# Performance work log

Measured on AMD Instinct MI355X. Metric: run time of the kernel, lower is better.

Reference implementation:

```python
import jax, jax.numpy as jnp
import numpy as np

H = 12  # num_heads

def _alibi_bias(num_heads, n, dtype):
    # slopes: ratio**i for i in 1..H, ratio = 2**(-8/H)
    ratio = 2.0 ** (-8.0 / num_heads)
    slopes = ratio ** jnp.arange(1, num_heads + 1, dtype=jnp.float32)  # [H]
    pos = jnp.arange(n)
    rel = jnp.abs(pos[None, :] - pos[:, None]).astype(jnp.float32)  # [N,N]
    return (-slopes[:, None, None] * rel[None]).astype(dtype)  # [H,N,N]

def setup_inputs() -> dict:
    key = jax.random.key(0)
    ks = jax.random.split(key, 5)
    B, N, C = 16, 1024, 768
    s = 0.02
    return {
        "x": jax.random.normal(ks[0], (B, N, C), jnp.float32),
        "w_qkv": jax.random.normal(ks[1], (3 * C, C), jnp.float32) * s,
        "b_qkv": jax.random.normal(ks[2], (3 * C,), jnp.float32) * s,
        "w_proj": jax.random.normal(ks[3], (C, C), jnp.float32) * s,
        "b_proj": jax.random.normal(ks[4], (C,), jnp.float32) * s,
    }

def reference(x, w_qkv, b_qkv, w_proj, b_proj):
    B, N, C = x.shape
    D = C // H
    scale = D ** -0.5
    qkv = x @ w_qkv.T + b_qkv                       # [B,N,3C]
    qkv = qkv.reshape(B, N, 3, H, D)
    q = qkv[:, :, 0].transpose(0, 2, 1, 3)          # [B,H,N,D]
    k = qkv[:, :, 1].transpose(0, 2, 1, 3)
    v = qkv[:, :, 2].transpose(0, 2, 1, 3)
    bias = _alibi_bias(H, N, x.dtype)               # [H,N,N]
    scores = jnp.einsum('bhnd,bhmd->bhnm', q, k) * scale + bias[None]
    attn = jax.nn.softmax(scores, axis=-1)
    out = jnp.einsum('bhnm,bhmd->bhnd', attn, v)    # [B,H,N,D]
    out = out.transpose(0, 2, 1, 3).reshape(B, N, C)
    return out @ w_proj.T + b_proj
```

## Files before the change

### kernel.cpp

```cpp
#include <hip/hip_runtime.h>


typedef unsigned short u16;
typedef unsigned int u32;
typedef __attribute__((ext_vector_type(8))) short short8;
typedef __attribute__((ext_vector_type(4))) float f32x4;

__device__ __forceinline__ u16 f2bf(float f) {
    u32 u = __float_as_uint(f);
    u32 r = u + 0x7FFFu + ((u >> 16) & 1u);
    return (u16)(r >> 16);
}

__device__ __forceinline__ f32x4 mfma16(short8 a, short8 b, f32x4 c) {
    return __builtin_amdgcn_mfma_f32_16x16x32_bf16(a, b, c, 0, 0, 0);
}
__device__ __forceinline__ u32 cvtpk_bf16(float lo, float hi) {
    u32 r;
    asm("v_cvt_pk_bf16_f32 %0, %1, %2" : "=v"(r) : "v"(lo), "v"(hi));
    return r;
}

typedef __attribute__((address_space(1))) const unsigned int gu32_t;
typedef __attribute__((address_space(3))) unsigned int su32_t;
__device__ __forceinline__ void gl16(const u16* g, u16* s) {
    __builtin_amdgcn_global_load_lds((gu32_t*)g, (su32_t*)s, 16, 0, 0);
}

__global__ void cvt_all(const float* __restrict__ x, const float* __restrict__ wq,
                        const float* __restrict__ wp, u16* __restrict__ Xb,
                        u16* __restrict__ Wqkvb, u16* __restrict__ Wprojb) {
    int i = blockIdx.x * blockDim.x + threadIdx.x;
    int stride = gridDim.x * blockDim.x;
    for (int idx = i; idx < 3735552; idx += stride) {
        const float* src;
        u16* dst;
        int k;
        if (idx < 3145728) { src = x; dst = Xb; k = idx; }
        else if (idx < 3588096) { src = wq; dst = Wqkvb; k = idx - 3145728; }
        else { src = wp; dst = Wprojb; k = idx - 3588096; }
        float4 v = *(const float4*)(src + (size_t)k * 4);
        ushort4 o;
        o.x = f2bf(v.x); o.y = f2bf(v.y); o.z = f2bf(v.z); o.w = f2bf(v.w);
        *(ushort4*)(dst + (size_t)k * 4) = o;
    }
}

template <int EPI>
__global__ __launch_bounds__(256) void gemm_nt(
    const u16* __restrict__ A, const u16* __restrict__ Bw,
    const float* __restrict__ bias, u16* __restrict__ outb, float* __restrict__ outf,
    int nTilesN)
{
    constexpr int K = 768;
    constexpr int nkt = K / 32;
    __shared__ __align__(16) u16 lA[3][128 * 32];
    __shared__ __align__(16) u16 lB[3][128 * 32];

    int tid = threadIdx.x;
    int bid = blockIdx.x;
    int nwg = gridDim.x;
    int cpx = nwg >> 3;
    int swz = (bid & 7) * cpx + (bid >> 3);
    int bm = swz / nTilesN;
    int bn = swz - bm * nTilesN;
    int m0 = bm * 128, n0 = bn * 128;

    int sr = tid >> 2;
    int sc = (tid & 3) << 3;
    const u16* pA = A + (size_t)(m0 + sr) * K + sc;
    const u16* pB = Bw + (size_t)(n0 + sr) * K + sc;
    int lo = tid * 8;

    gl16(pA, &lA[0][lo]);
    gl16(pA + (size_t)64 * K, &lA[0][lo + 2048]);
    gl16(pB, &lB[0][lo]);
    gl16(pB + (size_t)64 * K, &lB[0][lo + 2048]);
    gl16(pA + 32, &lA[1][lo]);
    gl16(pA + (size_t)64 * K + 32, &lA[1][lo + 2048]);
    gl16(pB + 32, &lB[1][lo]);
    gl16(pB + (size_t)64 * K + 32, &lB[1][lo + 2048]);

    int w = tid >> 6, lane = tid & 63;
    int wr = (w >> 1) << 6, wc = (w & 1) << 6;
    int fq = lane >> 4, fr = lane & 15;
    f32x4 acc[4][4] = {};

    for (int kt = 0; kt < nkt; ++kt) {
        int cur = kt % 3;
        if (kt < nkt - 1) { asm volatile("s_waitcnt vmcnt(4)" ::: "memory"); }
        else              { asm volatile("s_waitcnt vmcnt(0)" ::: "memory"); }
        __builtin_amdgcn_sched_barrier(0);
        __builtin_amdgcn_s_barrier();
        __builtin_amdgcn_sched_barrier(0);
        if (kt + 2 < nkt) {
            int nx = (kt + 2) % 3;
            const u16* qA = pA + (kt + 2) * 32;
            const u16* qB = pB + (kt + 2) * 32;
            gl16(qA, &lA[nx][lo]);
            gl16(qA + (size_t)64 * K, &lA[nx][lo + 2048]);
            gl16(qB, &lB[nx][lo]);
            gl16(qB + (size_t)64 * K, &lB[nx][lo + 2048]);
        }
        short8 af[4], bfr[4];
#pragma unroll
        for (int i = 0; i < 4; ++i)
            af[i] = *(const short8*)&lA[cur][(wr + i * 16 + fr) * 32 + fq * 8];
#pragma unroll
        for (int j = 0; j < 4; ++j)
            bfr[j] = *(const short8*)&lB[cur][(wc + j * 16 + fr) * 32 + fq * 8];
        __builtin_amdgcn_s_setprio(1);
#pragma unroll
        for (int i = 0; i < 4; ++i)
#pragma unroll
            for (int j = 0; j < 4; ++j)
                acc[i][j] = mfma16(af[i], bfr[j], acc[i][j]);
        __builtin_amdgcn_s_setprio(0);
    }

    if (EPI == 0) {
        int nbase = n0 + wc;
        int s = nbase / 768;
        int hh = (nbase % 768) >> 6;
        int b = m0 >> 10;
        int i0 = (m0 & 1023) + wr;
        u16* obase = outb + (((size_t)s * 16 + b) * 12 + hh) * 1024 * 64;
#pragma unroll
        for (int j = 0; j < 4; ++j) {
            float bval = bias[nbase + j * 16 + fr];
            int d = j * 16 + fr;
#pragma unroll
            for (int i = 0; i < 4; ++i) {
                int r0 = i0 + i * 16 + fq * 4;
#pragma unroll
                for (int r = 0; r < 4; ++r)
                    obase[(size_t)(r0 + r) * 64 + d] = f2bf(acc[i][j][r] + bval);
            }
        }
    } else {
#pragma unroll
        for (int j = 0; j < 4; ++j) {
            int col = n0 + wc + j * 16 + fr;
            float bval = bias[col];
#pragma unroll
            for (int i = 0; i < 4; ++i) {
                int row0 = m0 + wr + i * 16 + fq * 4;
#pragma unroll
                for (int r = 0; r < 4; ++r)
                    outf[(size_t)(row0 + r) * 768 + col] = acc[i][j][r] + bval;
            }
        }
    }
}

__global__ __launch_bounds__(256) void attn_alibi(
    const u16* __restrict__ QKV, u16* __restrict__ att)
{
    int g = blockIdx.x;
    int xcd = g & 7;
    int idx = g >> 3;
    int qt = idx & 15;
    int bh = xcd * 24 + (idx >> 4);
    int h = bh % 12;
    int b = bh / 12;
    int q0 = qt * 64;
    const u16* Qg = QKV + (size_t)bh * 65536;
    const u16* Kg = QKV + (size_t)(192 + bh) * 65536;
    const u16* Vg = QKV + (size_t)(384 + bh) * 65536;

    __shared__ __align__(16) u16 Qs[64][72];
    __shared__ __align__(16) u16 Ks[64][72];
    __shared__ __align__(16) u16 Vt[64][72];
    __shared__ __align__(16) u16 Ps[64][72];

    int tid = threadIdx.x, w = tid >> 6, lane = tid & 63;
    int fq = lane >> 4, fr = lane & 15;

    for (int c = tid; c < 512; c += 256) {
        int r = c >> 3, d = (c & 7) * 8;
        *(uint4*)&Qs[r][d] = *(const uint4*)(Qg + (size_t)(q0 + r) * 64 + d);
    }
    __syncthreads();
    short8 aq0 = *(const short8*)&Qs[w * 16 + fr][fq * 8];
    short8 aq1 = *(const short8*)&Qs[w * 16 + fr][32 + fq * 8];

    const float C1 = 0.125f * 1.44269504f;
    float c2 = __builtin_amdgcn_exp2f(-(2.0f / 3.0f) * (float)(h + 1)) * 1.44269504f;
    int distThr = (int)(40.0f / c2);
    int lo_kv = q0 - 63 - distThr;
    int hi_kv = q0 + 63 + distThr;
    int t_lo = (lo_kv <= 0) ? 0 : (lo_kv >> 6);
    int t_hi = (hi_kv >= 1023) ? 15 : (hi_kv >> 6);

    int sr0 = tid >> 3;
    int sr1 = sr0 + 32;
    int sc = (tid & 7) * 8;
    int vswz = (tid & 7) << 3;

    uint4 kr0 = *(const uint4*)(Kg + (size_t)(t_lo * 64 + sr0) * 64 + sc);
    uint4 kr1 = *(const uint4*)(Kg + (size_t)(t_lo * 64 + sr1) * 64 + sc);
    uint4 vr0 = *(const uint4*)(Vg + (size_t)(t_lo * 64 + sr0) * 64 + sc);
    uint4 vr1 = *(const uint4*)(Vg + (size_t)(t_lo * 64 + sr1) * 64 + sc);

    float di = (float)(q0 + w * 16 + fr - fq * 4);
    float lsum = 0.f;
    f32x4 acc[4] = {};

    for (int it = t_lo; it <= t_hi; ++it) {
        __syncthreads();
        *(uint4*)&Ks[sr0][sc] = kr0;
        *(uint4*)&Ks[sr1][sc] = kr1;
        {
            const u16* v0 = (const u16*)&vr0;
            const u16* v1 = (const u16*)&vr1;
#pragma unroll
            for (int jj = 0; jj < 8; ++jj) {
                Vt[sc + jj][sr0 ^ vswz] = v0[jj];
                Vt[sc + jj][sr1 ^ vswz] = v1[jj];
            }
        }
        __syncthreads();

        if (it < t_hi) {
            int kvn = (it + 1) * 64;
            kr0 = *(const uint4*)(Kg + (size_t)(kvn + sr0) * 64 + sc);
            kr1 = *(const uint4*)(Kg + (size_t)(kvn + sr1) * 64 + sc);
            vr0 = *(const uint4*)(Vg + (size_t)(kvn + sr0) * 64 + sc);
            vr1 = *(const uint4*)(Vg + (size_t)(kvn + sr1) * 64 + sc);
        }

        f32x4 sfr[4];
        __builtin_amdgcn_s_setprio(1);
#pragma unroll
        for (int ct = 0; ct < 4; ++ct) {
            short8 bk0 = *(const short8*)&Ks[ct * 16 + fr][fq * 8];
            short8 bk1 = *(const short8*)&Ks[ct * 16 + fr][32 + fq * 8];
            f32x4 s0 = {0.f, 0.f, 0.f, 0.f};
            s0 = mfma16(bk0, aq0, s0);
            s0 = mfma16(bk1, aq1, s0);
            sfr[ct] = s0;
        }
        __builtin_amdgcn_s_setprio(0);

        float dkv = di - (float)(it * 64);
#pragma unroll
        for (int ct = 0; ct < 4; ++ct) {
#pragma unroll
            for (int rp = 0; rp < 2; ++rp) {
                float t0 = dkv - (float)(ct * 16 + rp * 2);
                float e0 = __builtin_amdgcn_exp2f(fmaf(sfr[ct][rp * 2], C1, -c2 * fabsf(t0)));
                float e1 = __builtin_amdgcn_exp2f(fmaf(sfr[ct][rp * 2 + 1], C1, -c2 * fabsf(t0 - 1.0f)));
                lsum += e0 + e1;
                *(u32*)&Ps[w * 16 + fr][ct * 16 + fq * 4 + rp * 2] = cvtpk_bf16(e0, e1);
            }
        }

        short8 pa0 = *(const short8*)&Ps[w * 16 + fr][fq * 8];
        short8 pa1 = *(const short8*)&Ps[w * 16 + fr][32 + fq * 8];
        __builtin_amdgcn_s_setprio(1);
#pragma unroll
        for (int dt = 0; dt < 4; ++dt) {
            int row = dt * 16 + fr;
            int swzr = (row >> 3) << 3;
            short8 bv0 = *(const short8*)&Vt[row][(fq * 8) ^ swzr];
            short8 bv1 = *(const short8*)&Vt[row][(32 + fq * 8) ^ swzr];
            acc[dt] = mfma16(pa0, bv0, acc[dt]);
            acc[dt] = mfma16(pa1, bv1, acc[dt]);
        }
        __builtin_amdgcn_s_setprio(0);
    }

    float l = lsum;
    l += __shfl_xor(l, 16);
    l += __shfl_xor(l, 32);
    float rlo = 1.0f / l;
    float rl[4];
#pragma unroll
    for (int r = 0; r < 4; ++r)
        rl[r] = __shfl(rlo, fq * 4 + r);

#pragma unroll
    for (int dt = 0; dt < 4; ++dt)
#pragma unroll
        for (int r = 0; r < 4; ++r) {
            int ig = q0 + w * 16 + fq * 4 + r;
            att[((size_t)(b * 1024 + ig) * 12 + h) * 64 + dt * 16 + fr] =
                (u16)cvtpk_bf16(acc[dt][r] * rl[r], 0.f);
        }
}

extern "C" void kernel_launch(void* const* d_in, const int* in_sizes, int n_in,
                              void* d_out, int out_size, void* d_ws, size_t ws_size,
                              hipStream_t stream) {
    const float* x      = (const float*)d_in[0];
    const float* w_qkv  = (const float*)d_in[1];
    const float* b_qkv  = (const float*)d_in[2];
    const float* w_proj = (const float*)d_in[3];
    const float* b_proj = (const float*)d_in[4];
    float* out = (float*)d_out;

    char* ws = (char*)d_ws;
    u16* Xb     = (u16*)ws;
    u16* Wqkvb  = (u16*)(ws + 25165824);
    u16* Wprojb = (u16*)(ws + 28704768);
    u16* QKVb   = (u16*)(ws + 29884416);
    u16* Attb   = Xb;

    cvt_all<<<2048, 256, 0, stream>>>(x, w_qkv, w_proj, Xb, Wqkvb, Wprojb);

    gemm_nt<0><<<128 * 18, 256, 0, stream>>>(Xb, Wqkvb, b_qkv, QKVb, nullptr, 18);
    attn_alibi<<<3072, 256, 0, stream>>>(QKVb, Attb);
    gemm_nt<1><<<128 * 6, 256, 0, stream>>>(Attb, Wprojb, b_proj, nullptr, out, 6);
}
```

Before: 204.2 us.

## Enlarge GEMM M-tile to 256 and pack V-transpose and P stores

```diff
diff --git a/kernel.cpp b/kernel.cpp
--- a/kernel.cpp
+++ b/kernel.cpp
@@ -54,7 +54,7 @@
 {
     constexpr int K = 768;
     constexpr int nkt = K / 32;
-    __shared__ __align__(16) u16 lA[3][128 * 32];
+    __shared__ __align__(16) u16 lA[3][256 * 32];
     __shared__ __align__(16) u16 lB[3][128 * 32];
 
     int tid = threadIdx.x;
@@ -64,7 +64,7 @@
     int swz = (bid & 7) * cpx + (bid >> 3);
     int bm = swz / nTilesN;
     int bn = swz - bm * nTilesN;
-    int m0 = bm * 128, n0 = bn * 128;
+    int m0 = bm * 256, n0 = bn * 128;
 
     int sr = tid >> 2;
     int sc = (tid & 3) << 3;
@@ -72,23 +72,26 @@
     const u16* pB = Bw + (size_t)(n0 + sr) * K + sc;
     int lo = tid * 8;
 
-    gl16(pA, &lA[0][lo]);
-    gl16(pA + (size_t)64 * K, &lA[0][lo + 2048]);
-    gl16(pB, &lB[0][lo]);
-    gl16(pB + (size_t)64 * K, &lB[0][lo + 2048]);
-    gl16(pA + 32, &lA[1][lo]);
-    gl16(pA + (size_t)64 * K + 32, &lA[1][lo + 2048]);
-    gl16(pB + 32, &lB[1][lo]);
-    gl16(pB + (size_t)64 * K + 32, &lB[1][lo + 2048]);
+#pragma unroll
+    for (int t = 0; t < 2; ++t) {
+        const u16* qA = pA + t * 32;
+        const u16* qB = pB + t * 32;
+        gl16(qA,                     &lA[t][lo]);
+        gl16(qA + (size_t)64  * K,   &lA[t][lo + 2048]);
+        gl16(qA + (size_t)128 * K,   &lA[t][lo + 4096]);
+        gl16(qA + (size_t)192 * K,   &lA[t][lo + 6144]);
+        gl16(qB,                     &lB[t][lo]);
+        gl16(qB + (size_t)64  * K,   &lB[t][lo + 2048]);
+    }
 
     int w = tid >> 6, lane = tid & 63;
-    int wr = (w >> 1) << 6, wc = (w & 1) << 6;
+    int wm = w >> 1, wn = w & 1;
     int fq = lane >> 4, fr = lane & 15;
-    f32x4 acc[4][4] = {};
+    f32x4 acc[8][4] = {};
 
     for (int kt = 0; kt < nkt; ++kt) {
         int cur = kt % 3;
-        if (kt < nkt - 1) { asm volatile("s_waitcnt vmcnt(4)" ::: "memory"); }
+        if (kt < nkt - 1) { asm volatile("s_waitcnt vmcnt(6)" ::: "memory"); }
         else              { asm volatile("s_waitcnt vmcnt(0)" ::: "memory"); }
         __builtin_amdgcn_sched_barrier(0);
         __builtin_amdgcn_s_barrier();
@@ -97,21 +100,23 @@
             int nx = (kt + 2) % 3;
             const u16* qA = pA + (kt + 2) * 32;
             const u16* qB = pB + (kt + 2) * 32;
-            gl16(qA, &lA[nx][lo]);
-            gl16(qA + (size_t)64 * K, &lA[nx][lo + 2048]);
-            gl16(qB, &lB[nx][lo]);
-            gl16(qB + (size_t)64 * K, &lB[nx][lo + 2048]);
-        }
-        short8 af[4], bfr[4];
-#pragma unroll
-        for (int i = 0; i < 4; ++i)
-            af[i] = *(const short8*)&lA[cur][(wr + i * 16 + fr) * 32 + fq * 8];
+            gl16(qA,                     &lA[nx][lo]);
+            gl16(qA + (size_t)64  * K,   &lA[nx][lo + 2048]);
+            gl16(qA + (size_t)128 * K,   &lA[nx][lo + 4096]);
+            gl16(qA + (size_t)192 * K,   &lA[nx][lo + 6144]);
+            gl16(qB,                     &lB[nx][lo]);
+            gl16(qB + (size_t)64  * K,   &lB[nx][lo + 2048]);
+        }
+        short8 af[8], bfr[4];
+#pragma unroll
+        for (int i = 0; i < 8; ++i)
+            af[i] = *(const short8*)&lA[cur][(wm * 128 + i * 16 + fr) * 32 + fq * 8];
 #pragma unroll
         for (int j = 0; j < 4; ++j)
-            bfr[j] = *(const short8*)&lB[cur][(wc + j * 16 + fr) * 32 + fq * 8];
+            bfr[j] = *(const short8*)&lB[cur][(wn * 64 + j * 16 + fr) * 32 + fq * 8];
         __builtin_amdgcn_s_setprio(1);
 #pragma unroll
-        for (int i = 0; i < 4; ++i)
+        for (int i = 0; i < 8; ++i)
 #pragma unroll
             for (int j = 0; j < 4; ++j)
                 acc[i][j] = mfma16(af[i], bfr[j], acc[i][j]);
@@ -119,18 +124,18 @@
     }
 
     if (EPI == 0) {
-        int nbase = n0 + wc;
+        int nbase = n0 + wn * 64;
         int s = nbase / 768;
         int hh = (nbase % 768) >> 6;
         int b = m0 >> 10;
-        int i0 = (m0 & 1023) + wr;
+        int i0 = (m0 & 1023) + wm * 128;
         u16* obase = outb + (((size_t)s * 16 + b) * 12 + hh) * 1024 * 64;
 #pragma unroll
         for (int j = 0; j < 4; ++j) {
             float bval = bias[nbase + j * 16 + fr];
             int d = j * 16 + fr;
 #pragma unroll
-            for (int i = 0; i < 4; ++i) {
+            for (int i = 0; i < 8; ++i) {
                 int r0 = i0 + i * 16 + fq * 4;
 #pragma unroll
                 for (int r = 0; r < 4; ++r)
@@ -140,11 +145,11 @@
     } else {
 #pragma unroll
         for (int j = 0; j < 4; ++j) {
-            int col = n0 + wc + j * 16 + fr;
+            int col = n0 + wn * 64 + j * 16 + fr;
             float bval = bias[col];
 #pragma unroll
-            for (int i = 0; i < 4; ++i) {
-                int row0 = m0 + wr + i * 16 + fq * 4;
+            for (int i = 0; i < 8; ++i) {
+                int row0 = m0 + wm * 128 + i * 16 + fq * 4;
 #pragma unroll
                 for (int r = 0; r < 4; ++r)
                     outf[(size_t)(row0 + r) * 768 + col] = acc[i][j][r] + bval;
@@ -194,13 +199,14 @@
 
     int sr0 = tid >> 3;
     int sr1 = sr0 + 32;
+    int vk0 = sr0 * 2;
     int sc = (tid & 7) * 8;
     int vswz = (tid & 7) << 3;
 
     uint4 kr0 = *(const uint4*)(Kg + (size_t)(t_lo * 64 + sr0) * 64 + sc);
     uint4 kr1 = *(const uint4*)(Kg + (size_t)(t_lo * 64 + sr1) * 64 + sc);
-    uint4 vr0 = *(const uint4*)(Vg + (size_t)(t_lo * 64 + sr0) * 64 + sc);
-    uint4 vr1 = *(const uint4*)(Vg + (size_t)(t_lo * 64 + sr1) * 64 + sc);
+    uint4 vr0 = *(const uint4*)(Vg + (size_t)(t_lo * 64 + vk0) * 64 + sc);
+    uint4 vr1 = *(const uint4*)(Vg + (size_t)(t_lo * 64 + vk0 + 1) * 64 + sc);
 
     float di = (float)(q0 + w * 16 + fr - fq * 4);
     float lsum = 0.f;
@@ -213,11 +219,10 @@
         {
             const u16* v0 = (const u16*)&vr0;
             const u16* v1 = (const u16*)&vr1;
-#pragma unroll
-            for (int jj = 0; jj < 8; ++jj) {
-                Vt[sc + jj][sr0 ^ vswz] = v0[jj];
-                Vt[sc + jj][sr1 ^ vswz] = v1[jj];
-            }
+            int col = vk0 ^ vswz;
+#pragma unroll
+            for (int jj = 0; jj < 8; ++jj)
+                *(u32*)&Vt[sc + jj][col] = (u32)v0[jj] | ((u32)v1[jj] << 16);
         }
         __syncthreads();
 
@@ -225,8 +230,8 @@
             int kvn = (it + 1) * 64;
             kr0 = *(const uint4*)(Kg + (size_t)(kvn + sr0) * 64 + sc);
             kr1 = *(const uint4*)(Kg + (size_t)(kvn + sr1) * 64 + sc);
-            vr0 = *(const uint4*)(Vg + (size_t)(kvn + sr0) * 64 + sc);
-            vr1 = *(const uint4*)(Vg + (size_t)(kvn + sr1) * 64 + sc);
+            vr0 = *(const uint4*)(Vg + (size_t)(kvn + vk0) * 64 + sc);
+            vr1 = *(const uint4*)(Vg + (size_t)(kvn + vk0 + 1) * 64 + sc);
         }
 
         f32x4 sfr[4];
@@ -245,14 +250,16 @@
         float dkv = di - (float)(it * 64);
 #pragma unroll
         for (int ct = 0; ct < 4; ++ct) {
-#pragma unroll
-            for (int rp = 0; rp < 2; ++rp) {
-                float t0 = dkv - (float)(ct * 16 + rp * 2);
-                float e0 = __builtin_amdgcn_exp2f(fmaf(sfr[ct][rp * 2], C1, -c2 * fabsf(t0)));
-                float e1 = __builtin_amdgcn_exp2f(fmaf(sfr[ct][rp * 2 + 1], C1, -c2 * fabsf(t0 - 1.0f)));
-                lsum += e0 + e1;
-                *(u32*)&Ps[w * 16 + fr][ct * 16 + fq * 4 + rp * 2] = cvtpk_bf16(e0, e1);
-            }
+            float t0 = dkv - (float)(ct * 16);
+            float e0 = __builtin_amdgcn_exp2f(fmaf(sfr[ct][0], C1, -c2 * fabsf(t0)));
+            float e1 = __builtin_amdgcn_exp2f(fmaf(sfr[ct][1], C1, -c2 * fabsf(t0 - 1.0f)));
+            float e2 = __builtin_amdgcn_exp2f(fmaf(sfr[ct][2], C1, -c2 * fabsf(t0 - 2.0f)));
+            float e3 = __builtin_amdgcn_exp2f(fmaf(sfr[ct][3], C1, -c2 * fabsf(t0 - 3.0f)));
+            lsum += (e0 + e1) + (e2 + e3);
+            uint2 pk;
+            pk.x = cvtpk_bf16(e0, e1);
+            pk.y = cvtpk_bf16(e2, e3);
+            *(uint2*)&Ps[w * 16 + fr][ct * 16 + fq * 4] = pk;
         }
 
         short8 pa0 = *(const short8*)&Ps[w * 16 + fr][fq * 8];
@@ -308,7 +315,7 @@
 
     cvt_all<<<2048, 256, 0, stream>>>(x, w_qkv, w_proj, Xb, Wqkvb, Wprojb);
 
-    gemm_nt<0><<<128 * 18, 256, 0, stream>>>(Xb, Wqkvb, b_qkv, QKVb, nullptr, 18);
+    gemm_nt<0><<<64 * 18, 256, 0, stream>>>(Xb, Wqkvb, b_qkv, QKVb, nullptr, 18);
     attn_alibi<<<3072, 256, 0, stream>>>(QKVb, Attb);
-    gemm_nt<1><<<128 * 6, 256, 0, stream>>>(Attb, Wprojb, b_proj, nullptr, out, 6);
-}
+    gemm_nt<1><<<64 * 6, 256, 0, stream>>>(Attb, Wprojb, b_proj, nullptr, out, 6);
+}
```

Result: slower. 231.8 us (+13.5%).
